# Kernel optimization log

Measured on AMD Instinct MI355X. Metric: run time of the kernel, lower is better.

## Reference

```python
import jax, jax.numpy as jnp
import numpy as np

N, D = 1024, 128
NEG_INF = -1e30


def setup_inputs() -> dict:
    key = jax.random.key(0)
    ks = jax.random.split(key, 8)
    s = 0.05
    return {
        "X": jax.random.normal(ks[0], (N, D), dtype=jnp.float32),
        "Wq": jax.random.normal(ks[1], (D, D), dtype=jnp.float32) * s,
        "Wk": jax.random.normal(ks[2], (D, D), dtype=jnp.float32) * s,
        "v": jax.random.normal(ks[3], (D,), dtype=jnp.float32) * s,
        "w_ih": jax.random.normal(ks[4], (3 * D, 2 * D), dtype=jnp.float32) * s,
        "w_hh": jax.random.normal(ks[5], (3 * D, D), dtype=jnp.float32) * s,
        "b_ih": jax.random.normal(ks[6], (3 * D,), dtype=jnp.float32) * s,
        "b_hh": jax.random.normal(ks[7], (3 * D,), dtype=jnp.float32) * s,
    }


def reference(X, Wq, Wk, v, w_ih, w_hh, b_ih, b_hh):
    n, d = X.shape
    # --- anti-causal additive attention (query i attends keys j >= i) ---
    q = X @ Wq.T                                   # (N, d)
    k = X @ Wk.T                                   # (N, d)
    # scores[i, j] = v . tanh(q_i + k_j)
    scores = jnp.einsum("ijd,d->ij", jnp.tanh(q[:, None, :] + k[None, :, :]), v)
    mask = jnp.arange(n)[None, :] >= jnp.arange(n)[:, None]   # suffix j >= i
    scores = jnp.where(mask, scores, NEG_INF)
    w = jax.nn.softmax(scores, axis=1)             # (N, N)
    att = w @ X                                    # (N, d) context over keys

    # --- single-layer GRU over the N "time" steps, batch 1 ---
    gru_in = jnp.concatenate((X, att), axis=1)     # (N, 2d)
    gi = gru_in @ w_ih.T + b_ih                    # (N, 3d) input gates, precomputed

    def step(h, gi_t):
        gh = h @ w_hh.T + b_hh                     # (3d,)
        i_r, i_z, i_n = jnp.split(gi_t, 3)
        h_r, h_z, h_n = jnp.split(gh, 3)
        r = jax.nn.sigmoid(i_r + h_r)
        z = jax.nn.sigmoid(i_z + h_z)
        nst = jnp.tanh(i_n + r * h_n)
        h_new = (1.0 - z) * nst + z * h
        return h_new, h_new

    h0 = jnp.zeros((d,), dtype=X.dtype)
    _, out = jax.lax.scan(step, h0, gi)            # (N, d)
    return out
```

## Files before the change

### kernel.cpp

```cpp
#include <hip/hip_runtime.h>
#include <hip/hip_bf16.h>

#define N 1024
#define D 128
#define SB 32
#define NSB (N / SB)

typedef __hip_bfloat16 bf16;
typedef __attribute__((ext_vector_type(8))) short bfx8;
typedef __attribute__((ext_vector_type(4))) float fx4;
typedef __attribute__((ext_vector_type(8))) unsigned short u16x8;

__device__ __forceinline__ float b2f(bf16 x) { return __bfloat162float(x); }
__device__ __forceinline__ short f2bf_bits(float x) {
    bf16 b = __float2bfloat16(x);
    return *reinterpret_cast<short*>(&b);
}
__device__ __forceinline__ float bfbits2f(unsigned short u) {
    return __uint_as_float(((unsigned int)u) << 16);
}
__device__ __forceinline__ float fastrcp(float x) { return __builtin_amdgcn_rcpf(x); }

__device__ __forceinline__ float fast_tanh(float x) {
    float e = __expf(2.f * x);
    return 1.f - 2.f * fastrcp(e + 1.f);
}
__device__ __forceinline__ float fast_sigmoid(float x) {
    return fastrcp(1.f + __expf(-x));
}

__device__ __forceinline__ float sel4(fx4 v, int r) {
    float x = (r & 1) ? v[1] : v[0];
    float y = (r & 1) ? v[3] : v[2];
    return (r & 2) ? y : x;
}

__device__ __forceinline__ void async_copy16(const float* g, void* l) {
    __builtin_amdgcn_global_load_lds((const __attribute__((address_space(1))) void*)g,
                                     (__attribute__((address_space(3))) void*)l, 16, 0, 0);
}

__global__ void sniff_kernel(const unsigned short* __restrict__ xu, int* __restrict__ flag) {
    int l = threadIdx.x;
    int cnt = 0;
#pragma unroll
    for (int k = 0; k < 8; ++k) {
        unsigned short u = xu[2 * (l * 8 + k)];
        int e = (u >> 7) & 0xFF;
        cnt += (e >= 96 && e <= 144) ? 1 : 0;
    }
    for (int off = 32; off > 0; off >>= 1) cnt += __shfl_down(cnt, off);
    if (l == 0) *flag = (cnt > 400) ? 1 : 0;
}

struct ConvArgs {
    const void* p[8];
    float* o[8];
    int n[8];
};
__global__ void convert_kernel(ConvArgs A, const int* __restrict__ flag) {
    int seg = blockIdx.y;
    int n = A.n[seg];
    int isbf = *flag;
    const void* p = A.p[seg];
    float* o = A.o[seg];
    for (int i = blockIdx.x * blockDim.x + threadIdx.x; i < n; i += gridDim.x * blockDim.x) {
        float v = isbf ? b2f(((const bf16*)p)[i]) : ((const float*)p)[i];
        o[i] = v;
    }
}

__global__ void transpose_wih(const float* __restrict__ wih, float* __restrict__ wihT) {
    int id = blockIdx.x * 256 + threadIdx.x;
    int c = id / 384;
    int o = id - c * 384;
    wihT[id] = wih[o * 256 + c];
}

__global__ void qk_kernel(const float* __restrict__ X, const float* __restrict__ Wq,
                          const float* __restrict__ Wk,
                          float* __restrict__ q, float* __restrict__ kT) {
    int i = blockIdx.x & (N - 1);
    bool is_k = blockIdx.x >= N;
    int d = threadIdx.x;
    const float* W = is_k ? Wk : Wq;
    float acc = 0.f;
#pragma unroll 8
    for (int c = 0; c < D; ++c)
        acc += X[i * D + c] * W[d * D + c];
    if (is_k) kT[d * N + i] = acc;
    else      q[i * D + d] = acc;
}

__global__ void __launch_bounds__(256) attn_kernel(const float* __restrict__ q,
                                                   const float* __restrict__ kT,
                                                   const float* __restrict__ v,
                                                   const float* __restrict__ X,
                                                   const float* __restrict__ wihT,
                                                   const float* __restrict__ b_ih,
                                                   float* __restrict__ gi) {
    int i = blockIdx.x;
    __shared__ float qs[D], vs[D], xr[D], al[D];
    __shared__ float wrow[N];
    __shared__ float red[256];
    int t = threadIdx.x;
    if (t < D) { qs[t] = q[i * D + t]; vs[t] = v[t]; xr[t] = X[i * D + t]; }
    __syncthreads();

    float sj[4];
    int cnt = 0;
    float m = -1e30f;
    for (int j = i + t; j < N; j += 256) {
        float s = 0.f;
#pragma unroll 8
        for (int d = 0; d < D; ++d) s += vs[d] * fast_tanh(qs[d] + kT[d * N + j]);
        sj[cnt++] = s;
        m = fmaxf(m, s);
    }
    red[t] = m;
    __syncthreads();
    for (int st = 128; st > 0; st >>= 1) {
        if (t < st) red[t] = fmaxf(red[t], red[t + st]);
        __syncthreads();
    }
    m = red[0];
    __syncthreads();
    float lsum = 0.f;
    {
        int it = 0;
        for (int j = i + t; j < N; j += 256, ++it) {
            float p = __expf(sj[it] - m);
            wrow[j] = p;
            lsum += p;
        }
    }
    red[t] = lsum;
    __syncthreads();
    for (int st = 128; st > 0; st >>= 1) {
        if (t < st) red[t] += red[t + st];
        __syncthreads();
    }
    float inv = fastrcp(red[0]);
    __syncthreads();

    int d = t & 127, half = t >> 7;
    float acc = 0.f;
    for (int j = i + half; j < N; j += 2) acc += wrow[j] * X[j * D + d];
    if (half) red[d] = acc;
    __syncthreads();
    if (!half) al[d] = (acc + red[d]) * inv;
    __syncthreads();

    for (int o = t; o < 3 * D; o += 256) {
        float a2 = b_ih[o];
        const float* wt = wihT + o;
#pragma unroll 8
        for (int c = 0; c < D; ++c) a2 += xr[c] * wt[c * 384];
#pragma unroll 8
        for (int c = 0; c < D; ++c) a2 += al[c] * wt[(D + c) * 384];
        gi[i * 3 * D + o] = a2;
    }
}

__global__ void __launch_bounds__(256, 1) gru_kernel(const float* __restrict__ gi,
                                                     const float* __restrict__ w_hh,
                                                     const float* __restrict__ b_hh,
                                                     void* __restrict__ out,
                                                     const int* __restrict__ flag) {
    __shared__ float gi_lds[2][SB][3 * D];
    __shared__ short hist[SB + 1][D];
    int t = threadIdx.x;
    int w = t >> 6;
    int l = t & 63;
    int q = l >> 4;
    int nn = l & 15;
    int isbf = *flag;

    bfx8 a[3][2][4];
#pragma unroll
    for (int tau = 0; tau < 3; ++tau)
#pragma unroll
        for (int mqi = 0; mqi < 2; ++mqi)
#pragma unroll
            for (int kc = 0; kc < 4; ++kc) {
                int row = 128 * tau + 16 * (2 * w + mqi) + nn;
                int k0 = 32 * kc + 8 * q;
#pragma unroll
                for (int j = 0; j < 8; ++j)
                    a[tau][mqi][kc][j] = f2bf_bits(w_hh[row * D + k0 + j]);
            }
    fx4 bias[3][2];
#pragma unroll
    for (int tau = 0; tau < 3; ++tau)
#pragma unroll
        for (int mqi = 0; mqi < 2; ++mqi)
#pragma unroll
            for (int r = 0; r < 4; ++r)
                bias[tau][mqi][r] = b_hh[128 * tau + 16 * (2 * w + mqi) + 4 * q + r];

    int rsel = l & 3;
    int mqsel = (l >> 3) & 1;
    int drow = 32 * w + 16 * mqsel + 4 * q + rsel;
    float h = 0.f;

    int fr = 1 + (t >> 3);
    int fc = (t & 7) * 16;

    {
        const float* src = gi;
        for (int mm = 0; mm < 12; ++mm) {
            int off = (w * 12 + mm) * 256;
            async_copy16(src + off + (l << 2), (char*)&gi_lds[0][0][0] + off * 4);
        }
    }

    for (int sb = 0; sb < NSB; ++sb) {
        int cb = sb & 1;
        if (sb == 0) {
            if (t < 64) ((int*)&hist[0][0])[t] = 0;
        } else {
            u16x8 h0 = *(const u16x8*)&hist[fr][fc];
            u16x8 h1 = *(const u16x8*)&hist[fr][fc + 8];
            int orow = (sb - 1) * SB + fr - 1;
            if (isbf) {
                *(u16x8*)((unsigned short*)out + orow * D + fc) = h0;
                *(u16x8*)((unsigned short*)out + orow * D + fc + 8) = h1;
            } else {
                float* op = (float*)out + orow * D + fc;
                fx4 f0, f1, f2, f3;
#pragma unroll
                for (int j = 0; j < 4; ++j) {
                    f0[j] = bfbits2f(h0[j]);     f1[j] = bfbits2f(h0[4 + j]);
                    f2[j] = bfbits2f(h1[j]);     f3[j] = bfbits2f(h1[4 + j]);
                }
                *(fx4*)op = f0; *(fx4*)(op + 4) = f1;
                *(fx4*)(op + 8) = f2; *(fx4*)(op + 12) = f3;
            }
            if (t < 64) ((int*)&hist[0][0])[t] = ((const int*)&hist[SB][0])[t];
        }
        asm volatile("s_waitcnt vmcnt(0) lgkmcnt(0)\ns_barrier" ::: "memory");

        if (sb + 1 < NSB) {
            const float* src = gi + (size_t)(sb + 1) * SB * 3 * D;
            for (int mm = 0; mm < 12; ++mm) {
                int off = (w * 12 + mm) * 256;
                async_copy16(src + off + (l << 2), (char*)&gi_lds[cb ^ 1][0][0] + off * 4);
            }
        }

        const char* hrd = (const char*)&hist[0][0] + 16 * q;
        const float* gp = &gi_lds[cb][0][0] + drow;
        short* hwr = &hist[1][0] + drow;

        for (int s = 0; s < SB; ++s) {
            bfx8 b0 = *(const bfx8*)(hrd);
            bfx8 b1 = *(const bfx8*)(hrd + 64);
            bfx8 b2 = *(const bfx8*)(hrd + 128);
            bfx8 b3 = *(const bfx8*)(hrd + 192);
            float gr = gp[0];
            float gz = gp[D];
            float gn = gp[2 * D];

            fx4 acc[3][2];
#pragma unroll
            for (int tau = 0; tau < 3; ++tau)
#pragma unroll
                for (int mqi = 0; mqi < 2; ++mqi) {
                    fx4 c = bias[tau][mqi];
                    c = __builtin_amdgcn_mfma_f32_16x16x32_bf16(a[tau][mqi][0], b0, c, 0, 0, 0);
                    c = __builtin_amdgcn_mfma_f32_16x16x32_bf16(a[tau][mqi][1], b1, c, 0, 0, 0);
                    c = __builtin_amdgcn_mfma_f32_16x16x32_bf16(a[tau][mqi][2], b2, c, 0, 0, 0);
                    c = __builtin_amdgcn_mfma_f32_16x16x32_bf16(a[tau][mqi][3], b3, c, 0, 0, 0);
                    acc[tau][mqi] = c;
                }

            float ar = sel4(mqsel ? acc[0][1] : acc[0][0], rsel);
            float az = sel4(mqsel ? acc[1][1] : acc[1][0], rsel);
            float an = sel4(mqsel ? acc[2][1] : acc[2][0], rsel);
            float rr = fast_sigmoid(gr + ar);
            float zz = fast_sigmoid(gz + az);
            float nst = fast_tanh(gn + rr * an);
            h = (1.f - zz) * nst + zz * h;
            *hwr = f2bf_bits(h);

            hrd += 256;
            gp += 3 * D;
            hwr += D;
            asm volatile("s_waitcnt lgkmcnt(0)\ns_barrier" ::: "memory");
        }
    }
    {
        u16x8 h0 = *(const u16x8*)&hist[fr][fc];
        u16x8 h1 = *(const u16x8*)&hist[fr][fc + 8];
        int orow = (NSB - 1) * SB + fr - 1;
        if (isbf) {
            *(u16x8*)((unsigned short*)out + orow * D + fc) = h0;
            *(u16x8*)((unsigned short*)out + orow * D + fc + 8) = h1;
        } else {
            float* op = (float*)out + orow * D + fc;
            fx4 f0, f1, f2, f3;
#pragma unroll
            for (int j = 0; j < 4; ++j) {
                f0[j] = bfbits2f(h0[j]);     f1[j] = bfbits2f(h0[4 + j]);
                f2[j] = bfbits2f(h1[j]);     f3[j] = bfbits2f(h1[4 + j]);
            }
            *(fx4*)op = f0; *(fx4*)(op + 4) = f1;
            *(fx4*)(op + 8) = f2; *(fx4*)(op + 12) = f3;
        }
    }
}

extern "C" void kernel_launch(void* const* d_in, const int* in_sizes, int n_in,
                              void* d_out, int out_size, void* d_ws, size_t ws_size,
                              hipStream_t stream) {
    (void)in_sizes; (void)n_in; (void)out_size; (void)ws_size;

    float* w0 = (float*)d_ws;
    int*   flag = (int*)w0;
    float* Xf   = w0 + 16;
    float* Wqf  = Xf   + N * D;
    float* Wkf  = Wqf  + D * D;
    float* vf   = Wkf  + D * D;
    float* wihf = vf   + D;
    float* whhf = wihf + 3 * D * 2 * D;
    float* bihf = whhf + 3 * D * D;
    float* bhhf = bihf + 3 * D;
    float* q    = bhhf + 3 * D;
    float* kT   = q    + N * D;
    float* wihT = kT   + N * D;
    float* gi   = wihT + 3 * D * 2 * D;

    sniff_kernel<<<1, 64, 0, stream>>>((const unsigned short*)d_in[0], flag);

    ConvArgs A;
    A.p[0] = d_in[0]; A.o[0] = Xf;   A.n[0] = N * D;
    A.p[1] = d_in[1]; A.o[1] = Wqf;  A.n[1] = D * D;
    A.p[2] = d_in[2]; A.o[2] = Wkf;  A.n[2] = D * D;
    A.p[3] = d_in[3]; A.o[3] = vf;   A.n[3] = D;
    A.p[4] = d_in[4]; A.o[4] = wihf; A.n[4] = 3 * D * 2 * D;
    A.p[5] = d_in[5]; A.o[5] = whhf; A.n[5] = 3 * D * D;
    A.p[6] = d_in[6]; A.o[6] = bihf; A.n[6] = 3 * D;
    A.p[7] = d_in[7]; A.o[7] = bhhf; A.n[7] = 3 * D;
    dim3 cgrid(128, 8, 1);
    convert_kernel<<<cgrid, 256, 0, stream>>>(A, flag);

    transpose_wih<<<(3 * D * 2 * D) / 256, 256, 0, stream>>>(wihf, wihT);
    qk_kernel<<<2 * N, D, 0, stream>>>(Xf, Wqf, Wkf, q, kT);
    attn_kernel<<<N, 256, 0, stream>>>(q, kT, vf, Xf, wihT, bihf, gi);
    gru_kernel<<<1, 256, 0, stream>>>(gi, whhf, bhhf, d_out, flag);
}
```

Measured before the change: 632.8 us.

## Replace MFMA recurrent matvec with register-resident fp16 dot2 per-thread GRU step

```diff
diff --git a/kernel.cpp b/kernel.cpp
--- a/kernel.cpp
+++ b/kernel.cpp
@@ -7,14 +7,14 @@
 #define NSB (N / SB)
 
 typedef __hip_bfloat16 bf16;
-typedef __attribute__((ext_vector_type(8))) short bfx8;
+typedef __attribute__((ext_vector_type(2))) _Float16 f16x2;
 typedef __attribute__((ext_vector_type(4))) float fx4;
 typedef __attribute__((ext_vector_type(8))) unsigned short u16x8;
 
 __device__ __forceinline__ float b2f(bf16 x) { return __bfloat162float(x); }
-__device__ __forceinline__ short f2bf_bits(float x) {
+__device__ __forceinline__ unsigned short f2bf_bits(float x) {
     bf16 b = __float2bfloat16(x);
-    return *reinterpret_cast<short*>(&b);
+    return *reinterpret_cast<unsigned short*>(&b);
 }
 __device__ __forceinline__ float bfbits2f(unsigned short u) {
     return __uint_as_float(((unsigned int)u) << 16);
@@ -29,10 +29,12 @@
     return fastrcp(1.f + __expf(-x));
 }
 
-__device__ __forceinline__ float sel4(fx4 v, int r) {
-    float x = (r & 1) ? v[1] : v[0];
-    float y = (r & 1) ? v[3] : v[2];
-    return (r & 2) ? y : x;
+__device__ __forceinline__ float fdot2(f16x2 a, f16x2 b, float c) {
+#if __has_builtin(__builtin_amdgcn_fdot2)
+    return __builtin_amdgcn_fdot2(a, b, c, false);
+#else
+    return fmaf((float)a[0], (float)b[0], fmaf((float)a[1], (float)b[1], c));
+#endif
 }
 
 __device__ __forceinline__ void async_copy16(const float* g, void* l) {
@@ -168,60 +170,44 @@
                                                      void* __restrict__ out,
                                                      const int* __restrict__ flag) {
     __shared__ float gi_lds[2][SB][3 * D];
-    __shared__ short hist[SB + 1][D];
+    __shared__ f16x2 hcur[2][D / 2];
+    __shared__ unsigned short obuf[SB][D];
     int t = threadIdx.x;
-    int w = t >> 6;
-    int l = t & 63;
-    int q = l >> 4;
-    int nn = l & 15;
+    int d = t >> 1;
+    int half = t & 1;
     int isbf = *flag;
 
-    bfx8 a[3][2][4];
-#pragma unroll
-    for (int tau = 0; tau < 3; ++tau)
-#pragma unroll
-        for (int mqi = 0; mqi < 2; ++mqi)
-#pragma unroll
-            for (int kc = 0; kc < 4; ++kc) {
-                int row = 128 * tau + 16 * (2 * w + mqi) + nn;
-                int k0 = 32 * kc + 8 * q;
-#pragma unroll
-                for (int j = 0; j < 8; ++j)
-                    a[tau][mqi][kc][j] = f2bf_bits(w_hh[row * D + k0 + j]);
-            }
-    fx4 bias[3][2];
-#pragma unroll
-    for (int tau = 0; tau < 3; ++tau)
-#pragma unroll
-        for (int mqi = 0; mqi < 2; ++mqi)
-#pragma unroll
-            for (int r = 0; r < 4; ++r)
-                bias[tau][mqi][r] = b_hh[128 * tau + 16 * (2 * w + mqi) + 4 * q + r];
-
-    int rsel = l & 3;
-    int mqsel = (l >> 3) & 1;
-    int drow = 32 * w + 16 * mqsel + 4 * q + rsel;
+    f16x2 wr[32], wz[32], wn[32];
+    {
+        const float* wb = w_hh + 64 * half;
+#pragma unroll
+        for (int j = 0; j < 32; ++j) {
+            wr[j] = f16x2{(_Float16)wb[d * D + 2 * j], (_Float16)wb[d * D + 2 * j + 1]};
+            wz[j] = f16x2{(_Float16)wb[(d + D) * D + 2 * j], (_Float16)wb[(d + D) * D + 2 * j + 1]};
+            wn[j] = f16x2{(_Float16)wb[(d + 2 * D) * D + 2 * j], (_Float16)wb[(d + 2 * D) * D + 2 * j + 1]};
+        }
+    }
+    float br = b_hh[d], bz = b_hh[D + d], bn = b_hh[2 * D + d];
     float h = 0.f;
 
-    int fr = 1 + (t >> 3);
+    int fr = t >> 3;
     int fc = (t & 7) * 16;
 
     {
-        const float* src = gi;
         for (int mm = 0; mm < 12; ++mm) {
-            int off = (w * 12 + mm) * 256;
-            async_copy16(src + off + (l << 2), (char*)&gi_lds[0][0][0] + off * 4);
+            int off = ((t >> 6) * 12 + mm) * 256;
+            async_copy16(gi + off + ((t & 63) << 2), (char*)&gi_lds[0][0][0] + off * 4);
         }
     }
 
     for (int sb = 0; sb < NSB; ++sb) {
         int cb = sb & 1;
         if (sb == 0) {
-            if (t < 64) ((int*)&hist[0][0])[t] = 0;
+            if (t < 64) ((int*)&hcur[0][0])[t] = 0;
         } else {
-            u16x8 h0 = *(const u16x8*)&hist[fr][fc];
-            u16x8 h1 = *(const u16x8*)&hist[fr][fc + 8];
-            int orow = (sb - 1) * SB + fr - 1;
+            u16x8 h0 = *(const u16x8*)&obuf[fr][fc];
+            u16x8 h1 = *(const u16x8*)&obuf[fr][fc + 8];
+            int orow = (sb - 1) * SB + fr;
             if (isbf) {
                 *(u16x8*)((unsigned short*)out + orow * D + fc) = h0;
                 *(u16x8*)((unsigned short*)out + orow * D + fc + 8) = h1;
@@ -236,63 +222,63 @@
                 *(fx4*)op = f0; *(fx4*)(op + 4) = f1;
                 *(fx4*)(op + 8) = f2; *(fx4*)(op + 12) = f3;
             }
-            if (t < 64) ((int*)&hist[0][0])[t] = ((const int*)&hist[SB][0])[t];
         }
         asm volatile("s_waitcnt vmcnt(0) lgkmcnt(0)\ns_barrier" ::: "memory");
 
         if (sb + 1 < NSB) {
             const float* src = gi + (size_t)(sb + 1) * SB * 3 * D;
             for (int mm = 0; mm < 12; ++mm) {
-                int off = (w * 12 + mm) * 256;
-                async_copy16(src + off + (l << 2), (char*)&gi_lds[cb ^ 1][0][0] + off * 4);
-            }
-        }
-
-        const char* hrd = (const char*)&hist[0][0] + 16 * q;
-        const float* gp = &gi_lds[cb][0][0] + drow;
-        short* hwr = &hist[1][0] + drow;
+                int off = ((t >> 6) * 12 + mm) * 256;
+                async_copy16(src + off + ((t & 63) << 2), (char*)&gi_lds[cb ^ 1][0][0] + off * 4);
+            }
+        }
+
+        const float* gp = &gi_lds[cb][0][0] + d;
 
         for (int s = 0; s < SB; ++s) {
-            bfx8 b0 = *(const bfx8*)(hrd);
-            bfx8 b1 = *(const bfx8*)(hrd + 64);
-            bfx8 b2 = *(const bfx8*)(hrd + 128);
-            bfx8 b3 = *(const bfx8*)(hrd + 192);
+            int pp = s & 1;
+            union { fx4 v4[8]; f16x2 h2[32]; } hu;
+            {
+                const fx4* hp4 = (const fx4*)&hcur[pp][half * 32];
+#pragma unroll
+                for (int j = 0; j < 8; ++j) hu.v4[j] = hp4[j];
+            }
             float gr = gp[0];
             float gz = gp[D];
             float gn = gp[2 * D];
 
-            fx4 acc[3][2];
-#pragma unroll
-            for (int tau = 0; tau < 3; ++tau)
-#pragma unroll
-                for (int mqi = 0; mqi < 2; ++mqi) {
-                    fx4 c = bias[tau][mqi];
-                    c = __builtin_amdgcn_mfma_f32_16x16x32_bf16(a[tau][mqi][0], b0, c, 0, 0, 0);
-                    c = __builtin_amdgcn_mfma_f32_16x16x32_bf16(a[tau][mqi][1], b1, c, 0, 0, 0);
-                    c = __builtin_amdgcn_mfma_f32_16x16x32_bf16(a[tau][mqi][2], b2, c, 0, 0, 0);
-                    c = __builtin_amdgcn_mfma_f32_16x16x32_bf16(a[tau][mqi][3], b3, c, 0, 0, 0);
-                    acc[tau][mqi] = c;
-                }
-
-            float ar = sel4(mqsel ? acc[0][1] : acc[0][0], rsel);
-            float az = sel4(mqsel ? acc[1][1] : acc[1][0], rsel);
-            float an = sel4(mqsel ? acc[2][1] : acc[2][0], rsel);
-            float rr = fast_sigmoid(gr + ar);
-            float zz = fast_sigmoid(gz + az);
-            float nst = fast_tanh(gn + rr * an);
+            float r0 = 0.f, r1 = 0.f, z0 = 0.f, z1 = 0.f, n0 = 0.f, n1 = 0.f;
+#pragma unroll
+            for (int j = 0; j < 16; ++j) {
+                r0 = fdot2(wr[j], hu.h2[j], r0);
+                r1 = fdot2(wr[j + 16], hu.h2[j + 16], r1);
+                z0 = fdot2(wz[j], hu.h2[j], z0);
+                z1 = fdot2(wz[j + 16], hu.h2[j + 16], z1);
+                n0 = fdot2(wn[j], hu.h2[j], n0);
+                n1 = fdot2(wn[j + 16], hu.h2[j + 16], n1);
+            }
+            float sr = r0 + r1, sz = z0 + z1, sn = n0 + n1;
+            sr += __shfl_xor(sr, 1);
+            sz += __shfl_xor(sz, 1);
+            sn += __shfl_xor(sn, 1);
+
+            float rr = fast_sigmoid(gr + sr + br);
+            float zz = fast_sigmoid(gz + sz + bz);
+            float nst = fast_tanh(gn + rr * (sn + bn));
             h = (1.f - zz) * nst + zz * h;
-            *hwr = f2bf_bits(h);
-
-            hrd += 256;
+
+            if (!half) {
+                ((_Float16*)&hcur[pp ^ 1][0])[d] = (_Float16)h;
+                obuf[s][d] = f2bf_bits(h);
+            }
             gp += 3 * D;
-            hwr += D;
             asm volatile("s_waitcnt lgkmcnt(0)\ns_barrier" ::: "memory");
         }
     }
     {
-        u16x8 h0 = *(const u16x8*)&hist[fr][fc];
-        u16x8 h1 = *(const u16x8*)&hist[fr][fc + 8];
-        int orow = (NSB - 1) * SB + fr - 1;
+        u16x8 h0 = *(const u16x8*)&obuf[fr][fc];
+        u16x8 h1 = *(const u16x8*)&obuf[fr][fc + 8];
+        int orow = (NSB - 1) * SB + fr;
         if (isbf) {
             *(u16x8*)((unsigned short*)out + orow * D + fc) = h0;
             *(u16x8*)((unsigned short*)out + orow * D + fc + 8) = h1;
```

After: 694.9 us. 9.8% more time.

## Fuse attention and GRU into one kernel with per-row readiness flags

Applied to the files above, without the earlier changes.

```diff
diff --git a/kernel.cpp b/kernel.cpp
--- a/kernel.cpp
+++ b/kernel.cpp
@@ -92,17 +92,29 @@
     else      q[i * D + d] = acc;
 }
 
-__global__ void __launch_bounds__(256) attn_kernel(const float* __restrict__ q,
-                                                   const float* __restrict__ kT,
-                                                   const float* __restrict__ v,
-                                                   const float* __restrict__ X,
-                                                   const float* __restrict__ wihT,
-                                                   const float* __restrict__ b_ih,
-                                                   float* __restrict__ gi) {
-    int i = blockIdx.x;
-    __shared__ float qs[D], vs[D], xr[D], al[D];
-    __shared__ float wrow[N];
-    __shared__ float red[256];
+#define SMEM_BYTES 106752
+
+__device__ __forceinline__ void wait_chunk(const int* rflag, int base, int t) {
+    if (t < SB) {
+        while (__hip_atomic_load(rflag + base + t, __ATOMIC_ACQUIRE,
+                                 __HIP_MEMORY_SCOPE_AGENT) == 0) {
+            __builtin_amdgcn_s_sleep(1);
+        }
+    }
+    __syncthreads();
+}
+
+__device__ void attn_body(char* smem, int i,
+                          const float* __restrict__ q, const float* __restrict__ kT,
+                          const float* __restrict__ v, const float* __restrict__ X,
+                          const float* __restrict__ wihT, const float* __restrict__ b_ih,
+                          float* __restrict__ gi, int* __restrict__ rflag) {
+    float* qs = (float*)smem;
+    float* vs = qs + D;
+    float* xr = vs + D;
+    float* al = xr + D;
+    float* wrow = al + D;
+    float* red = wrow + N;
     int t = threadIdx.x;
     if (t < D) { qs[t] = q[i * D + t]; vs[t] = v[t]; xr[t] = X[i * D + t]; }
     __syncthreads();
@@ -160,21 +172,23 @@
         for (int c = 0; c < D; ++c) a2 += al[c] * wt[(D + c) * 384];
         gi[i * 3 * D + o] = a2;
     }
-}
-
-__global__ void __launch_bounds__(256, 1) gru_kernel(const float* __restrict__ gi,
-                                                     const float* __restrict__ w_hh,
-                                                     const float* __restrict__ b_hh,
-                                                     void* __restrict__ out,
-                                                     const int* __restrict__ flag) {
-    __shared__ float gi_lds[2][SB][3 * D];
-    __shared__ short hist[SB + 1][D];
+    __threadfence();
+    __syncthreads();
+    if (t == 0) __hip_atomic_store(rflag + i, 1, __ATOMIC_RELEASE, __HIP_MEMORY_SCOPE_AGENT);
+}
+
+__device__ void gru_body(char* smem, const float* __restrict__ gi,
+                         const float* __restrict__ w_hh, const float* __restrict__ b_hh,
+                         void* __restrict__ out, const int* __restrict__ dflag,
+                         const int* __restrict__ rflag) {
+    float (*gi_lds)[SB][3 * D] = (float (*)[SB][3 * D])smem;
+    short (*hist)[D] = (short (*)[D])(smem + 98304);
     int t = threadIdx.x;
     int w = t >> 6;
     int l = t & 63;
     int q = l >> 4;
     int nn = l & 15;
-    int isbf = *flag;
+    int isbf = *dflag;
 
     bfx8 a[3][2][4];
 #pragma unroll
@@ -206,11 +220,11 @@
     int fr = 1 + (t >> 3);
     int fc = (t & 7) * 16;
 
+    wait_chunk(rflag, 0, t);
     {
-        const float* src = gi;
         for (int mm = 0; mm < 12; ++mm) {
             int off = (w * 12 + mm) * 256;
-            async_copy16(src + off + (l << 2), (char*)&gi_lds[0][0][0] + off * 4);
+            async_copy16(gi + off + (l << 2), (char*)&gi_lds[0][0][0] + off * 4);
         }
     }
 
@@ -241,6 +255,7 @@
         asm volatile("s_waitcnt vmcnt(0) lgkmcnt(0)\ns_barrier" ::: "memory");
 
         if (sb + 1 < NSB) {
+            wait_chunk(rflag, (sb + 1) * SB, t);
             const float* src = gi + (size_t)(sb + 1) * SB * 3 * D;
             for (int mm = 0; mm < 12; ++mm) {
                 int off = (w * 12 + mm) * 256;
@@ -310,14 +325,35 @@
     }
 }
 
+__global__ void __launch_bounds__(256, 1) mega_kernel(const float* __restrict__ q,
+                                                      const float* __restrict__ kT,
+                                                      const float* __restrict__ v,
+                                                      const float* __restrict__ X,
+                                                      const float* __restrict__ wihT,
+                                                      const float* __restrict__ b_ih,
+                                                      float* __restrict__ gi,
+                                                      const float* __restrict__ w_hh,
+                                                      const float* __restrict__ b_hh,
+                                                      void* __restrict__ out,
+                                                      const int* __restrict__ dflag,
+                                                      int* __restrict__ rflag) {
+    __shared__ __align__(16) char smem[SMEM_BYTES];
+    if (blockIdx.x != 0) {
+        attn_body(smem, (int)blockIdx.x - 1, q, kT, v, X, wihT, b_ih, gi, rflag);
+    } else {
+        gru_body(smem, gi, w_hh, b_hh, out, dflag, rflag);
+    }
+}
+
 extern "C" void kernel_launch(void* const* d_in, const int* in_sizes, int n_in,
                               void* d_out, int out_size, void* d_ws, size_t ws_size,
                               hipStream_t stream) {
     (void)in_sizes; (void)n_in; (void)out_size; (void)ws_size;
 
     float* w0 = (float*)d_ws;
-    int*   flag = (int*)w0;
-    float* Xf   = w0 + 16;
+    int*   dflag = (int*)w0;
+    int*   rflag = (int*)(w0 + 16);
+    float* Xf   = w0 + 16 + N;
     float* Wqf  = Xf   + N * D;
     float* Wkf  = Wqf  + D * D;
     float* vf   = Wkf  + D * D;
@@ -330,7 +366,8 @@
     float* wihT = kT   + N * D;
     float* gi   = wihT + 3 * D * 2 * D;
 
-    sniff_kernel<<<1, 64, 0, stream>>>((const unsigned short*)d_in[0], flag);
+    sniff_kernel<<<1, 64, 0, stream>>>((const unsigned short*)d_in[0], dflag);
+    hipMemsetAsync(rflag, 0, N * sizeof(int), stream);
 
     ConvArgs A;
     A.p[0] = d_in[0]; A.o[0] = Xf;   A.n[0] = N * D;
@@ -342,10 +379,10 @@
     A.p[6] = d_in[6]; A.o[6] = bihf; A.n[6] = 3 * D;
     A.p[7] = d_in[7]; A.o[7] = bhhf; A.n[7] = 3 * D;
     dim3 cgrid(128, 8, 1);
-    convert_kernel<<<cgrid, 256, 0, stream>>>(A, flag);
+    convert_kernel<<<cgrid, 256, 0, stream>>>(A, dflag);
 
     transpose_wih<<<(3 * D * 2 * D) / 256, 256, 0, stream>>>(wihf, wihT);
     qk_kernel<<<2 * N, D, 0, stream>>>(Xf, Wqf, Wkf, q, kT);
-    attn_kernel<<<N, 256, 0, stream>>>(q, kT, vf, Xf, wihT, bihf, gi);
-    gru_kernel<<<1, 256, 0, stream>>>(gi, whhf, bhhf, d_out, flag);
-}
+    mega_kernel<<<1 + N, 256, 0, stream>>>(q, kT, vf, Xf, wihT, bihf, gi,
+                                           whhf, bhhf, d_out, dflag, rflag);
+}
```

Measured after the change: 714.7 us. 12.9% more time.
